# Optimization experiments

Measured on AMD Instinct MI355X. Metric: run time of the kernel, lower is better.

Reference implementation:

```python
import jax, jax.numpy as jnp
import numpy as np

N = 100000      # nodes
E = 3200000     # edges (before self loops)
IN = 128        # in_channels
H = 8           # heads
C = 16          # out_channels per head
NEG_SLOPE = 0.2


def setup_inputs() -> dict:
    key = jax.random.key(0)
    k1, k2, k3, k4, k5, k6 = jax.random.split(key, 6)
    x = jax.random.normal(k1, (N, IN), dtype=jnp.float32)
    edge_index = jax.random.randint(k2, (2, E), 0, N, dtype=jnp.int32)
    # GATConv params: lin weight [IN, H*C], att_src/att_dst [H, C], bias [H*C]
    W = jax.random.normal(k3, (IN, H * C), dtype=jnp.float32) / np.float32(np.sqrt(IN))
    att_src = jax.random.normal(k4, (H, C), dtype=jnp.float32) / np.float32(np.sqrt(C))
    att_dst = jax.random.normal(k5, (H, C), dtype=jnp.float32) / np.float32(np.sqrt(C))
    bias = jax.random.normal(k6, (H * C,), dtype=jnp.float32) * 0.01
    return {"x": x, "edge_index": edge_index, "W": W,
            "att_src": att_src, "att_dst": att_dst, "bias": bias}


def reference(x, edge_index, W, att_src, att_dst, bias):
    n = x.shape[0]
    h = (x @ W).reshape(n, H, C)                      # [N, H, C]
    # add self loops (PyG default add_self_loops=True)
    loop = jnp.arange(n, dtype=edge_index.dtype)
    src = jnp.concatenate([edge_index[0], loop])      # [E+N] message sources j
    dst = jnp.concatenate([edge_index[1], loop])      # [E+N] targets i
    # per-node attention logits
    a_src = jnp.einsum('nhc,hc->nh', h, att_src)      # [N, H]
    a_dst = jnp.einsum('nhc,hc->nh', h, att_dst)      # [N, H]
    alpha = jax.nn.leaky_relu(a_src[src] + a_dst[dst], NEG_SLOPE)  # [E+N, H]
    # segment softmax over edges grouped by destination node
    amax = jax.lax.stop_gradient(jax.ops.segment_max(alpha, dst, num_segments=n))
    ex = jnp.exp(alpha - amax[dst])
    denom = jax.ops.segment_sum(ex, dst, num_segments=n)           # [N, H]
    w = ex / (denom[dst] + 1e-16)                                  # [E+N, H]
    msg = h[src] * w[:, :, None]                                   # [E+N, H, C]
    out = jax.ops.segment_sum(msg, dst, num_segments=n)            # [N, H, C]
    return out.reshape(n, H * C) + bias
```

## Files before the change

### kernel.cpp

```cpp
#include <hip/hip_runtime.h>
#include <hip/hip_bf16.h>

#define H 8
#define C 16
#define HC 128
#define NEG 0.2f
#define XS_S 132

#define ANSH 6
#define AN 64
#define AMSK 63
#define CAP 2560
#define MAXB 2048
#define EPB 8192

__device__ __forceinline__ float lrelu(float x) { return fmaxf(x, NEG * x); }

__device__ __forceinline__ unsigned pack_bf16(float a, float b) {
    union { __hip_bfloat16 h; unsigned short u; } ua, ub;
    ua.h = __float2bfloat16(a);
    ub.h = __float2bfloat16(b);
    return (unsigned)ua.u | ((unsigned)ub.u << 16);
}
__device__ __forceinline__ float bf_lo(unsigned d) { return __uint_as_float(d << 16); }
__device__ __forceinline__ float bf_hi(unsigned d) { return __uint_as_float(d & 0xffff0000u); }

__global__ void __launch_bounds__(256) k1_gemm(const float* __restrict__ x,
                                               const float* __restrict__ W,
                                               const float* __restrict__ att_src,
                                               const float* __restrict__ att_dst,
                                               unsigned* __restrict__ h16,
                                               float* __restrict__ a_src,
                                               float* __restrict__ a_dst, int N) {
    __shared__ float xs[64 * XS_S];
    const int n0 = blockIdx.x * 64;
    const int t = threadIdx.x;
#pragma unroll
    for (int i = 0; i < 8; ++i) {
        int id = t + 256 * i;
        int r = id >> 5, kq = id & 31;
        int n = n0 + r;
        float4 v = (n < N) ? ((const float4*)x)[(size_t)n * 32 + kq]
                           : make_float4(0.f, 0.f, 0.f, 0.f);
        *(float4*)&xs[r * XS_S + kq * 4] = v;
    }
    __syncthreads();
    const int cg = t & 31;
    const int r0 = (t >> 5) * 8;
    float acc[8][4];
#pragma unroll
    for (int i = 0; i < 8; ++i)
#pragma unroll
        for (int j = 0; j < 4; ++j) acc[i][j] = 0.f;

#pragma unroll 4
    for (int k = 0; k < HC; ++k) {
        const float4 wv = ((const float4*)W)[k * 32 + cg];
        float wr[4] = {wv.x, wv.y, wv.z, wv.w};
#pragma unroll
        for (int i = 0; i < 8; ++i) {
            float xv = xs[(r0 + i) * XS_S + k];
#pragma unroll
            for (int j = 0; j < 4; ++j) acc[i][j] += xv * wr[j];
        }
    }
    const int fhd = cg >> 2;
    const int cq  = cg & 3;
#pragma unroll
    for (int i = 0; i < 8; ++i) {
        int n = n0 + r0 + i;
        if (n < N) {
            uint2 dv = make_uint2(pack_bf16(acc[i][0], acc[i][1]),
                                  pack_bf16(acc[i][2], acc[i][3]));
            *(uint2*)&h16[(size_t)n * 64 + cg * 2] = dv;
        }
        float ps = 0.f, pd = 0.f;
#pragma unroll
        for (int jj = 0; jj < 4; ++jj) {
            float hv = acc[i][jj];
            ps += hv * att_src[fhd * C + cq * 4 + jj];
            pd += hv * att_dst[fhd * C + cq * 4 + jj];
        }
        ps += __shfl_xor(ps, 1, 4); pd += __shfl_xor(pd, 1, 4);
        ps += __shfl_xor(ps, 2, 4); pd += __shfl_xor(pd, 2, 4);
        if (cq == 0 && n < N) {
            a_src[(unsigned)n * 8u + fhd] = ps;
            a_dst[(unsigned)n * 8u + fhd] = pd;
        }
    }
}

__global__ void __launch_bounds__(512) kb_bin(const int* __restrict__ ei,
                                              int* __restrict__ gcount,
                                              unsigned* __restrict__ pairs,
                                              int E, int B) {
    __shared__ unsigned spairs[EPB];
    __shared__ int cnt[MAXB];
    __shared__ int scn[MAXB];
    __shared__ int gbase[MAXB];
    const int t = threadIdx.x;
    const int e0 = blockIdx.x * EPB;
    const int nE = min(EPB, E - e0);
    for (int i = t; i < B; i += 512) cnt[i] = 0;
    __syncthreads();

    const bool v4 = ((E & 3) == 0) && ((nE & 3) == 0);
    const int nE4 = nE >> 2;
    const int4* d4p = (const int4*)(ei + E + e0);
    const int4* s4p = (const int4*)(ei + e0);
    if (v4) {
        for (int i = t; i < nE4; i += 512) {
            int4 d = d4p[i];
            atomicAdd(&cnt[d.x >> ANSH], 1);
            atomicAdd(&cnt[d.y >> ANSH], 1);
            atomicAdd(&cnt[d.z >> ANSH], 1);
            atomicAdd(&cnt[d.w >> ANSH], 1);
        }
    } else {
        for (int i = t; i < nE; i += 512)
            atomicAdd(&cnt[ei[E + e0 + i] >> ANSH], 1);
    }
    __syncthreads();

    for (int i = t; i < MAXB; i += 512) scn[i] = (i < B) ? cnt[i] : 0;
    __syncthreads();
    for (int off = 1; off < MAXB; off <<= 1) {
        int i0 = t, i1 = t + 512, i2 = t + 1024, i3 = t + 1536;
        int v0 = (i0 >= off) ? scn[i0 - off] : 0;
        int v1 = (i1 >= off) ? scn[i1 - off] : 0;
        int v2 = (i2 >= off) ? scn[i2 - off] : 0;
        int v3 = (i3 >= off) ? scn[i3 - off] : 0;
        __syncthreads();
        scn[i0] += v0; scn[i1] += v1; scn[i2] += v2; scn[i3] += v3;
        __syncthreads();
    }

    for (int i = t; i < B; i += 512) {
        int h = cnt[i];
        if (h) gbase[i] = i * CAP + atomicAdd(&gcount[i], h);
        cnt[i] = scn[i] - h;
    }
    __syncthreads();

    if (v4) {
        for (int i = t; i < nE4; i += 512) {
            int4 d = d4p[i];
            int4 sv = s4p[i];
#pragma unroll
            for (int q = 0; q < 4; ++q) {
                int dst = (&d.x)[q], src = (&sv.x)[q];
                int bk = dst >> ANSH;
                int pos = atomicAdd(&cnt[bk], 1);
                spairs[pos] = (unsigned)src | ((unsigned)(dst & AMSK) << 18);
            }
        }
    } else {
        for (int i = t; i < nE; i += 512) {
            int dst = ei[E + e0 + i], src = ei[e0 + i];
            int bk = dst >> ANSH;
            int pos = atomicAdd(&cnt[bk], 1);
            spairs[pos] = (unsigned)src | ((unsigned)(dst & AMSK) << 18);
        }
    }
    __syncthreads();

    const int wv = t >> 6, lane = t & 63;
    for (int i = wv; i < B; i += 8) {
        int end = scn[i];
        int st  = (i > 0) ? scn[i - 1] : 0;
        int len = end - st;
        if (len <= 0) continue;
        int gb = gbase[i];
        int rem = i * CAP + CAP - gb;
        int wl = min(len, max(rem, 0));
        for (int k = lane; k < wl; k += 64)
            pairs[gb + k] = spairs[st + k];
    }
}

__global__ void __launch_bounds__(512) k_fused(const unsigned* __restrict__ pairs,
                                               const int* __restrict__ gcount,
                                               const unsigned* __restrict__ h16,
                                               const float* __restrict__ a_src,
                                               const float* __restrict__ a_dst,
                                               const float* __restrict__ bias,
                                               float* __restrict__ out, int N) {
    __shared__ int cnt[AN];
    __shared__ int sc[AN];
    __shared__ int lcur[AN];
    __shared__ int lbeg[AN + 1];
    __shared__ unsigned scol[CAP];
    const int b = blockIdx.x;
    const int t = threadIdx.x;
    const int n0 = b << ANSH;
    const unsigned base = (unsigned)b * (unsigned)CAP;
    const int cb = min(gcount[b], CAP);

    if (t < AN) cnt[t] = 0;
    __syncthreads();
    for (int j = t; j < cb; j += 512)
        atomicAdd(&cnt[pairs[base + j] >> 18], 1);
    __syncthreads();
    if (t < AN) sc[t] = cnt[t];
    __syncthreads();
    for (int off = 1; off < AN; off <<= 1) {
        int v = (t < AN && t >= off) ? sc[t - off] : 0;
        __syncthreads();
        if (t < AN) sc[t] += v;
        __syncthreads();
    }
    if (t < AN) {
        lbeg[t + 1] = sc[t];
        lcur[t] = sc[t] - cnt[t];
        if (t == 0) lbeg[0] = 0;
    }
    __syncthreads();
    for (int j = t; j < cb; j += 512) {
        unsigned pv = pairs[base + j];
        int pos = atomicAdd(&lcur[pv >> 18], 1);
        scol[pos] = pv & 0x3FFFFu;
    }
    __syncthreads();

    const int wv = t >> 6;
    const int lane = t & 63;
    const int hd = lane >> 3;
    const int hw = lane & 7;
    const int bidx = hd * 4;

    for (int nl = wv; nl < AN; nl += 8) {
        const int node = n0 + nl;
        if (node >= N) break;
        const float adst_own = a_dst[(unsigned)node * 8u + (unsigned)hd];
        const float adst_hh  = a_dst[(unsigned)node * 8u + (unsigned)hw];
        const float wself = __expf(lrelu(a_src[(unsigned)node * 8u + (unsigned)hd] + adst_own));
        unsigned dself = h16[(unsigned)node * 64u + (unsigned)lane];
        float a0 = bf_lo(dself) * wself, a1 = bf_hi(dself) * wself;
        float b0 = 0.f, b1 = 0.f, c0 = 0.f, c1 = 0.f, e0 = 0.f, e1 = 0.f;
        float sA = wself, sB = 0.f, sC = 0.f, sD = 0.f;

        const int beg = lbeg[nl], end = lbeg[nl + 1];
        int j = beg;
        for (; j + 8 <= end; j += 8) {
            unsigned m0 = scol[j],     m1 = scol[j + 1], m2 = scol[j + 2], m3 = scol[j + 3];
            unsigned m4 = scol[j + 4], m5 = scol[j + 5], m6 = scol[j + 6], m7 = scol[j + 7];
            unsigned nP = scol[j + (lane >> 3)];
            float wme = __expf(lrelu(a_src[nP * 8u + (unsigned)hw] + adst_hh));
            int wi = __float_as_int(wme);
            float w0 = __int_as_float(__builtin_amdgcn_ds_bpermute(bidx,       wi));
            float w1 = __int_as_float(__builtin_amdgcn_ds_bpermute(bidx + 32,  wi));
            float w2 = __int_as_float(__builtin_amdgcn_ds_bpermute(bidx + 64,  wi));
            float w3 = __int_as_float(__builtin_amdgcn_ds_bpermute(bidx + 96,  wi));
            float w4 = __int_as_float(__builtin_amdgcn_ds_bpermute(bidx + 128, wi));
            float w5 = __int_as_float(__builtin_amdgcn_ds_bpermute(bidx + 160, wi));
            float w6 = __int_as_float(__builtin_amdgcn_ds_bpermute(bidx + 192, wi));
            float w7 = __int_as_float(__builtin_amdgcn_ds_bpermute(bidx + 224, wi));
            unsigned d0 = h16[m0 * 64u + (unsigned)lane];
            unsigned d1 = h16[m1 * 64u + (unsigned)lane];
            unsigned d2 = h16[m2 * 64u + (unsigned)lane];
            unsigned d3 = h16[m3 * 64u + (unsigned)lane];
            unsigned d4 = h16[m4 * 64u + (unsigned)lane];
            unsigned d5 = h16[m5 * 64u + (unsigned)lane];
            unsigned d6 = h16[m6 * 64u + (unsigned)lane];
            unsigned d7 = h16[m7 * 64u + (unsigned)lane];
            a0 += bf_lo(d0) * w0; a1 += bf_hi(d0) * w0; sA += w0;
            b0 += bf_lo(d1) * w1; b1 += bf_hi(d1) * w1; sB += w1;
            c0 += bf_lo(d2) * w2; c1 += bf_hi(d2) * w2; sC += w2;
            e0 += bf_lo(d3) * w3; e1 += bf_hi(d3) * w3; sD += w3;
            a0 += bf_lo(d4) * w4; a1 += bf_hi(d4) * w4; sA += w4;
            b0 += bf_lo(d5) * w5; b1 += bf_hi(d5) * w5; sB += w5;
            c0 += bf_lo(d6) * w6; c1 += bf_hi(d6) * w6; sC += w6;
            e0 += bf_lo(d7) * w7; e1 += bf_hi(d7) * w7; sD += w7;
        }
        if (j + 4 <= end) {
            unsigned m0 = scol[j], m1 = scol[j + 1], m2 = scol[j + 2], m3 = scol[j + 3];
            unsigned nP = scol[j + ((lane >> 3) & 3)];
            float wme = __expf(lrelu(a_src[nP * 8u + (unsigned)hw] + adst_hh));
            int wi = __float_as_int(wme);
            float w0 = __int_as_float(__builtin_amdgcn_ds_bpermute(bidx,      wi));
            float w1 = __int_as_float(__builtin_amdgcn_ds_bpermute(bidx + 32, wi));
            float w2 = __int_as_float(__builtin_amdgcn_ds_bpermute(bidx + 64, wi));
            float w3 = __int_as_float(__builtin_amdgcn_ds_bpermute(bidx + 96, wi));
            unsigned d0 = h16[m0 * 64u + (unsigned)lane];
            unsigned d1 = h16[m1 * 64u + (unsigned)lane];
            unsigned d2 = h16[m2 * 64u + (unsigned)lane];
            unsigned d3 = h16[m3 * 64u + (unsigned)lane];
            a0 += bf_lo(d0) * w0; a1 += bf_hi(d0) * w0; sA += w0;
            b0 += bf_lo(d1) * w1; b1 += bf_hi(d1) * w1; sB += w1;
            c0 += bf_lo(d2) * w2; c1 += bf_hi(d2) * w2; sC += w2;
            e0 += bf_lo(d3) * w3; e1 += bf_hi(d3) * w3; sD += w3;
            j += 4;
        }
        for (; j < end; ++j) {
            unsigned mA = scol[j];
            float wA = __expf(lrelu(a_src[mA * 8u + (unsigned)hd] + adst_own));
            unsigned dA = h16[mA * 64u + (unsigned)lane];
            a0 += bf_lo(dA) * wA; a1 += bf_hi(dA) * wA; sA += wA;
        }
        const float s = sA + sB + sC + sD;
        const float inv = 1.f / (s + 1e-16f);
        const float acc0 = a0 + b0 + c0 + e0;
        const float acc1 = a1 + b1 + c1 + e1;
        const float2 bv = ((const float2*)bias)[lane];
        float2 o;
        o.x = acc0 * inv + bv.x;
        o.y = acc1 * inv + bv.y;
        ((float2*)out)[(unsigned)node * 64u + (unsigned)lane] = o;
    }
}

extern "C" void kernel_launch(void* const* d_in, const int* in_sizes, int n_in,
                              void* d_out, int out_size, void* d_ws, size_t ws_size,
                              hipStream_t stream) {
    const float* x       = (const float*)d_in[0];
    const int*   ei      = (const int*)d_in[1];
    const float* W       = (const float*)d_in[2];
    const float* att_src = (const float*)d_in[3];
    const float* att_dst = (const float*)d_in[4];
    const float* bias    = (const float*)d_in[5];
    float* out = (float*)d_out;

    const int N = in_sizes[0] / HC;
    const int E = in_sizes[1] / 2;
    const int B = (N + AMSK) >> ANSH;
    const int nbin = (E + EPB - 1) / EPB;

    unsigned* h16 = (unsigned*)d_ws;
    float* a_src  = (float*)(h16 + (size_t)N * 64);
    float* a_dst  = a_src + (size_t)N * H;
    int* gcount   = (int*)(a_dst + (size_t)N * H);
    unsigned* pairs = (unsigned*)(gcount + MAXB);

    static hipStream_t s_side = nullptr;
    static hipEvent_t ev_fork = nullptr, ev_join = nullptr;
    if (s_side == nullptr) {
        (void)hipStreamCreateWithFlags(&s_side, hipStreamNonBlocking);
        (void)hipEventCreateWithFlags(&ev_fork, hipEventDisableTiming);
        (void)hipEventCreateWithFlags(&ev_join, hipEventDisableTiming);
    }
    const bool fork = (s_side != nullptr && ev_fork != nullptr && ev_join != nullptr);
    hipStream_t sb = fork ? s_side : stream;

    if (fork) {
        (void)hipEventRecord(ev_fork, stream);
        (void)hipStreamWaitEvent(sb, ev_fork, 0);
    }

    (void)hipMemsetAsync(gcount, 0, MAXB * sizeof(int), sb);
    kb_bin<<<nbin, 512, 0, sb>>>(ei, gcount, pairs, E, B);
    if (fork) (void)hipEventRecord(ev_join, sb);

    k1_gemm<<<(N + 63) / 64, 256, 0, stream>>>(x, W, att_src, att_dst,
                                               h16, a_src, a_dst, N);

    if (fork) (void)hipStreamWaitEvent(stream, ev_join, 0);

    k_fused<<<B, 512, 0, stream>>>(pairs, gcount, h16, a_src,
                                   a_dst, bias, out, N);
}
```

Measured before the change: 411.6 us.

## Split edge binning into two-pass radix partition by destination

Replaces the single-pass binning into 1563 fine buckets with two passes: first into 25 coarse buckets of 4096 nodes, then each coarse bucket is split into 64 fine buckets of 64 nodes. The goal is to cut the per-block cost of scanning and allocating 2048 counters and to make global writes more contiguous. In exchange it adds an extra kernel and an extra round trip of the edge list through global memory, plus a larger workspace for the intermediate pairs.

```diff
diff --git a/kernel.cpp b/kernel.cpp
--- a/kernel.cpp
+++ b/kernel.cpp
@@ -10,8 +10,11 @@
 #define ANSH 6
 #define AN 64
 #define AMSK 63
-#define CAP 2560
-#define MAXB 2048
+#define CAP2 2560
+#define MAXB2 2048
+#define CB_SH 12
+#define CBMSK 4095
+#define MAXB1 64
 #define EPB 8192
 
 __device__ __forceinline__ float lrelu(float x) { return fmaxf(x, NEG * x); }
@@ -90,18 +93,18 @@
     }
 }
 
-__global__ void __launch_bounds__(512) kb_bin(const int* __restrict__ ei,
-                                              int* __restrict__ gcount,
-                                              unsigned* __restrict__ pairs,
-                                              int E, int B) {
-    __shared__ unsigned spairs[EPB];
-    __shared__ int cnt[MAXB];
-    __shared__ int scn[MAXB];
-    __shared__ int gbase[MAXB];
+__global__ void __launch_bounds__(512) kb_bin1(const int* __restrict__ ei,
+                                               int* __restrict__ gcount1,
+                                               unsigned* __restrict__ pairs1,
+                                               int E, int NB1, int cap1) {
+    __shared__ unsigned sp[EPB];
+    __shared__ int cnt[MAXB1];
+    __shared__ int scn[MAXB1];
+    __shared__ int gbase[MAXB1];
     const int t = threadIdx.x;
     const int e0 = blockIdx.x * EPB;
     const int nE = min(EPB, E - e0);
-    for (int i = t; i < B; i += 512) cnt[i] = 0;
+    if (t < MAXB1) cnt[t] = 0;
     __syncthreads();
 
     const bool v4 = ((E & 3) == 0) && ((nE & 3) == 0);
@@ -111,37 +114,30 @@
     if (v4) {
         for (int i = t; i < nE4; i += 512) {
             int4 d = d4p[i];
-            atomicAdd(&cnt[d.x >> ANSH], 1);
-            atomicAdd(&cnt[d.y >> ANSH], 1);
-            atomicAdd(&cnt[d.z >> ANSH], 1);
-            atomicAdd(&cnt[d.w >> ANSH], 1);
+            atomicAdd(&cnt[d.x >> CB_SH], 1);
+            atomicAdd(&cnt[d.y >> CB_SH], 1);
+            atomicAdd(&cnt[d.z >> CB_SH], 1);
+            atomicAdd(&cnt[d.w >> CB_SH], 1);
         }
     } else {
         for (int i = t; i < nE; i += 512)
-            atomicAdd(&cnt[ei[E + e0 + i] >> ANSH], 1);
-    }
-    __syncthreads();
-
-    for (int i = t; i < MAXB; i += 512) scn[i] = (i < B) ? cnt[i] : 0;
-    __syncthreads();
-    for (int off = 1; off < MAXB; off <<= 1) {
-        int i0 = t, i1 = t + 512, i2 = t + 1024, i3 = t + 1536;
-        int v0 = (i0 >= off) ? scn[i0 - off] : 0;
-        int v1 = (i1 >= off) ? scn[i1 - off] : 0;
-        int v2 = (i2 >= off) ? scn[i2 - off] : 0;
-        int v3 = (i3 >= off) ? scn[i3 - off] : 0;
-        __syncthreads();
-        scn[i0] += v0; scn[i1] += v1; scn[i2] += v2; scn[i3] += v3;
-        __syncthreads();
-    }
-
-    for (int i = t; i < B; i += 512) {
-        int h = cnt[i];
-        if (h) gbase[i] = i * CAP + atomicAdd(&gcount[i], h);
-        cnt[i] = scn[i] - h;
-    }
-    __syncthreads();
-
+            atomicAdd(&cnt[ei[E + e0 + i] >> CB_SH], 1);
+    }
+    __syncthreads();
+    if (t < MAXB1) scn[t] = cnt[t];
+    __syncthreads();
+    for (int off = 1; off < MAXB1; off <<= 1) {
+        int v = (t < MAXB1 && t >= off) ? scn[t - off] : 0;
+        __syncthreads();
+        if (t < MAXB1) scn[t] += v;
+        __syncthreads();
+    }
+    if (t < MAXB1) {
+        int h = cnt[t];
+        gbase[t] = h ? t * cap1 + atomicAdd(&gcount1[t], h) : 0;
+        cnt[t] = scn[t] - h;
+    }
+    __syncthreads();
     if (v4) {
         for (int i = t; i < nE4; i += 512) {
             int4 d = d4p[i];
@@ -149,32 +145,106 @@
 #pragma unroll
             for (int q = 0; q < 4; ++q) {
                 int dst = (&d.x)[q], src = (&sv.x)[q];
-                int bk = dst >> ANSH;
-                int pos = atomicAdd(&cnt[bk], 1);
-                spairs[pos] = (unsigned)src | ((unsigned)(dst & AMSK) << 18);
+                int pos = atomicAdd(&cnt[dst >> CB_SH], 1);
+                sp[pos] = (unsigned)src | ((unsigned)(dst & CBMSK) << 17);
             }
         }
     } else {
         for (int i = t; i < nE; i += 512) {
             int dst = ei[E + e0 + i], src = ei[e0 + i];
-            int bk = dst >> ANSH;
-            int pos = atomicAdd(&cnt[bk], 1);
-            spairs[pos] = (unsigned)src | ((unsigned)(dst & AMSK) << 18);
-        }
-    }
-    __syncthreads();
-
+            int pos = atomicAdd(&cnt[dst >> CB_SH], 1);
+            sp[pos] = (unsigned)src | ((unsigned)(dst & CBMSK) << 17);
+        }
+    }
+    __syncthreads();
     const int wv = t >> 6, lane = t & 63;
-    for (int i = wv; i < B; i += 8) {
+    for (int i = wv; i < NB1; i += 8) {
         int end = scn[i];
         int st  = (i > 0) ? scn[i - 1] : 0;
         int len = end - st;
         if (len <= 0) continue;
         int gb = gbase[i];
-        int rem = i * CAP + CAP - gb;
+        int rem = i * cap1 + cap1 - gb;
         int wl = min(len, max(rem, 0));
         for (int k = lane; k < wl; k += 64)
-            pairs[gb + k] = spairs[st + k];
+            pairs1[gb + k] = sp[st + k];
+    }
+}
+
+__global__ void __launch_bounds__(512) kb_bin2(const unsigned* __restrict__ pairs1,
+                                               const int* __restrict__ gcount1,
+                                               int* __restrict__ gcount2,
+                                               unsigned* __restrict__ pairs2,
+                                               int cap1, int ch2) {
+    __shared__ unsigned sp[EPB];
+    __shared__ int cnt[64];
+    __shared__ int scn[64];
+    __shared__ int gbase[64];
+    const int cb = blockIdx.x / ch2;
+    const int ci = blockIdx.x % ch2;
+    const int c1 = min(gcount1[cb], cap1);
+    const int e0 = ci * EPB;
+    if (e0 >= c1) return;
+    const int nE = min(EPB, c1 - e0);
+    const unsigned b1 = (unsigned)cb * (unsigned)cap1 + (unsigned)e0;
+    const int t = threadIdx.x;
+    if (t < 64) cnt[t] = 0;
+    __syncthreads();
+
+    const int nE4 = nE >> 2;
+    const uint4* p4 = (const uint4*)(pairs1 + b1);
+    for (int i = t; i < nE4; i += 512) {
+        uint4 p = p4[i];
+        atomicAdd(&cnt[p.x >> 23], 1);
+        atomicAdd(&cnt[p.y >> 23], 1);
+        atomicAdd(&cnt[p.z >> 23], 1);
+        atomicAdd(&cnt[p.w >> 23], 1);
+    }
+    for (int i = (nE4 << 2) + t; i < nE; i += 512)
+        atomicAdd(&cnt[pairs1[b1 + i] >> 23], 1);
+    __syncthreads();
+    if (t < 64) scn[t] = cnt[t];
+    __syncthreads();
+    for (int off = 1; off < 64; off <<= 1) {
+        int v = (t < 64 && t >= off) ? scn[t - off] : 0;
+        __syncthreads();
+        if (t < 64) scn[t] += v;
+        __syncthreads();
+    }
+    if (t < 64) {
+        int h = cnt[t];
+        int gfb = cb * 64 + t;
+        gbase[t] = h ? gfb * CAP2 + atomicAdd(&gcount2[gfb], h) : 0;
+        cnt[t] = scn[t] - h;
+    }
+    __syncthreads();
+    for (int i = t; i < nE4; i += 512) {
+        uint4 p = p4[i];
+#pragma unroll
+        for (int q = 0; q < 4; ++q) {
+            unsigned pv = (&p.x)[q];
+            int pos = atomicAdd(&cnt[pv >> 23], 1);
+            sp[pos] = (pv & 0x1FFFFu) | (((pv >> 17) & 63u) << 18);
+        }
+    }
+    for (int i = (nE4 << 2) + t; i < nE; i += 512) {
+        unsigned pv = pairs1[b1 + i];
+        int pos = atomicAdd(&cnt[pv >> 23], 1);
+        sp[pos] = (pv & 0x1FFFFu) | (((pv >> 17) & 63u) << 18);
+    }
+    __syncthreads();
+    const int wv = t >> 6, lane = t & 63;
+    for (int i = wv; i < 64; i += 8) {
+        int end = scn[i];
+        int st  = (i > 0) ? scn[i - 1] : 0;
+        int len = end - st;
+        if (len <= 0) continue;
+        int gb = gbase[i];
+        int fb0 = (cb * 64 + i) * CAP2;
+        int rem = fb0 + CAP2 - gb;
+        int wl = min(len, max(rem, 0));
+        for (int k = lane; k < wl; k += 64)
+            pairs2[gb + k] = sp[st + k];
     }
 }
 
@@ -189,12 +259,12 @@
     __shared__ int sc[AN];
     __shared__ int lcur[AN];
     __shared__ int lbeg[AN + 1];
-    __shared__ unsigned scol[CAP];
+    __shared__ unsigned scol[CAP2];
     const int b = blockIdx.x;
     const int t = threadIdx.x;
     const int n0 = b << ANSH;
-    const unsigned base = (unsigned)b * (unsigned)CAP;
-    const int cb = min(gcount[b], CAP);
+    const unsigned base = (unsigned)b * (unsigned)CAP2;
+    const int cb = min(gcount[b], CAP2);
 
     if (t < AN) cnt[t] = 0;
     __syncthreads();
@@ -323,13 +393,18 @@
     const int N = in_sizes[0] / HC;
     const int E = in_sizes[1] / 2;
     const int B = (N + AMSK) >> ANSH;
+    const int NB1 = (N + CBMSK) >> CB_SH;
     const int nbin = (E + EPB - 1) / EPB;
+    const int cap1 = (((E + NB1 - 1) / NB1) + 32768 + 3) & ~3;
+    const int ch2 = (cap1 + EPB - 1) / EPB;
 
     unsigned* h16 = (unsigned*)d_ws;
     float* a_src  = (float*)(h16 + (size_t)N * 64);
     float* a_dst  = a_src + (size_t)N * H;
-    int* gcount   = (int*)(a_dst + (size_t)N * H);
-    unsigned* pairs = (unsigned*)(gcount + MAXB);
+    int* gcount1  = (int*)(a_dst + (size_t)N * H);
+    int* gcount2  = gcount1 + MAXB1;
+    unsigned* pairs1 = (unsigned*)(gcount2 + MAXB2);
+    unsigned* pairs2 = pairs1 + (size_t)NB1 * (size_t)cap1;
 
     static hipStream_t s_side = nullptr;
     static hipEvent_t ev_fork = nullptr, ev_join = nullptr;
@@ -346,8 +421,10 @@
         (void)hipStreamWaitEvent(sb, ev_fork, 0);
     }
 
-    (void)hipMemsetAsync(gcount, 0, MAXB * sizeof(int), sb);
-    kb_bin<<<nbin, 512, 0, sb>>>(ei, gcount, pairs, E, B);
+    (void)hipMemsetAsync(gcount1, 0, (MAXB1 + MAXB2) * sizeof(int), sb);
+    kb_bin1<<<nbin, 512, 0, sb>>>(ei, gcount1, pairs1, E, NB1, cap1);
+    kb_bin2<<<NB1 * ch2, 512, 0, sb>>>(pairs1, gcount1, gcount2, pairs2,
+                                       cap1, ch2);
     if (fork) (void)hipEventRecord(ev_join, sb);
 
     k1_gemm<<<(N + 63) / 64, 256, 0, stream>>>(x, W, att_src, att_dst,
@@ -355,6 +432,6 @@
 
     if (fork) (void)hipStreamWaitEvent(stream, ev_join, 0);
 
-    k_fused<<<B, 512, 0, stream>>>(pairs, gcount, h16, a_src,
+    k_fused<<<B, 512, 0, stream>>>(pairs2, gcount2, h16, a_src,
                                    a_dst, bias, out, N);
 }
```

Measured after the change: 369.9 us. 1.11x faster.
